# Kernel optimization log

Hardware: AMD Instinct MI355X
Metric: run time of the kernel (lower is better)

## Reference

```python
import jax, jax.numpy as jnp
import numpy as np

D = 512; H = 8; DH = D // H; FFN = 2048; K = 31; N = 4; T = 1024


def _ln(x, g, b):
    m = jnp.mean(x, -1, keepdims=True)
    v = jnp.var(x, -1, keepdims=True)
    return (x - m) * jax.lax.rsqrt(v + 1e-5) * g + b


def _ff(x, g, b, w1, b1, w2, b2):
    h = jax.nn.silu(_ln(x, g, b) @ w1 + b1)
    return 0.5 * (h @ w2 + b2)


def _forward(x, rel_pe, ln1_g, ln1_b, ff1_w1, ff1_b1, ff1_w2, ff1_b2,
             an_g, an_b, wq, bq, wk, bk, wv, bv, wo, bo, pos_w, u, v,
             cn_g, cn_b, pe_w, pe_b, dw_w, dw_b, bn_g, bn_b, pc_w, pc_b,
             ln2_g, ln2_b, ff2_w1, ff2_b1, ff2_w2, ff2_b2, fn_g, fn_b):
    Nb, Tt, _ = x.shape
    # macaron FF 1 (half-step)
    x = x + _ff(x, ln1_g, ln1_b, ff1_w1, ff1_b1, ff1_w2, ff1_b2)

    # RPE multi-head attention (Transformer-XL style)
    xa = _ln(x, an_g, an_b)
    split = lambda m: m.reshape(Nb, Tt, H, DH).transpose(0, 2, 1, 3)  # (N,H,T,dh)
    Q = split(xa @ wq + bq)
    Kk = split(xa @ wk + bk)
    V = split(xa @ wv + bv)
    # content-to-content: (Q+u) K^T
    AC = jnp.einsum('nhtd,nhsd->nhts', Q + u[None, :, None, :], Kk)
    # content-to-position: (Q+v) R^T, then rel-shift gather
    R = (rel_pe @ pos_w).reshape(2 * Tt - 1, H, DH)  # (2T-1,H,dh)
    BD_raw = jnp.einsum('nhtd,phd->nhtp', Q + v[None, :, None, :], R)  # (N,H,T,2T-1)
    idx = jnp.arange(Tt - 1, -1, -1)[None, :] + jnp.arange(Tt)[:, None]  # (T,T): i-j+(T-1)
    BD = jnp.take_along_axis(BD_raw, idx[None, None, :, :], axis=-1)  # (N,H,T,T)
    scores = (AC + BD) * (DH ** -0.5)
    attn = jax.nn.softmax(scores, axis=-1)
    out = jnp.einsum('nhts,nhsd->nthd', attn, V).reshape(Nb, Tt, D)
    x = x + (out @ wo + bo)

    # conv module: LN -> pointwise expand -> GLU -> depthwise conv -> BN(eval) -> SiLU -> pointwise
    c = _ln(x, cn_g, cn_b) @ pe_w + pe_b  # (N,T,2D)
    a, g = jnp.split(c, 2, axis=-1)
    c = a * jax.nn.sigmoid(g)
    c = c.transpose(0, 2, 1)  # (N,D,T)
    c = jax.lax.conv_general_dilated(
        c, dw_w, window_strides=(1,), padding=[(K // 2, K // 2)],
        dimension_numbers=('NCH', 'OIH', 'NCH'), feature_group_count=D)
    c = c + dw_b[None, :, None]
    # BatchNorm1d in eval mode: running_mean=0, running_var=1
    c = c * bn_g[None, :, None] + bn_b[None, :, None]
    c = jax.nn.silu(c).transpose(0, 2, 1) @ pc_w + pc_b
    x = x + c

    # macaron FF 2 + final LN
    x = x + _ff(x, ln2_g, ln2_b, ff2_w1, ff2_b1, ff2_w2, ff2_b2)
    return _ln(x, fn_g, fn_b)


def setup_inputs() -> dict:
    keys = iter(jax.random.split(jax.random.key(0), 64))
    def rn(*shape, s=0.02):
        return jax.random.normal(next(keys), shape, jnp.float32) * s
    inp = {}
    inp['x'] = rn(N, T, D, s=1.0)
    inp['rel_pe'] = rn(2 * T - 1, D, s=1.0)
    inp['ln1_g'] = jnp.ones(D); inp['ln1_b'] = jnp.zeros(D)
    inp['ff1_w1'] = rn(D, FFN); inp['ff1_b1'] = jnp.zeros(FFN)
    inp['ff1_w2'] = rn(FFN, D); inp['ff1_b2'] = jnp.zeros(D)
    inp['an_g'] = jnp.ones(D); inp['an_b'] = jnp.zeros(D)
    inp['wq'] = rn(D, D); inp['bq'] = jnp.zeros(D)
    inp['wk'] = rn(D, D); inp['bk'] = jnp.zeros(D)
    inp['wv'] = rn(D, D); inp['bv'] = jnp.zeros(D)
    inp['wo'] = rn(D, D); inp['bo'] = jnp.zeros(D)
    inp['pos_w'] = rn(D, D)
    inp['u'] = rn(H, DH); inp['v'] = rn(H, DH)
    inp['cn_g'] = jnp.ones(D); inp['cn_b'] = jnp.zeros(D)
    inp['pe_w'] = rn(D, 2 * D); inp['pe_b'] = jnp.zeros(2 * D)
    inp['dw_w'] = rn(D, 1, K); inp['dw_b'] = jnp.zeros(D)
    inp['bn_g'] = jnp.ones(D); inp['bn_b'] = jnp.zeros(D)
    inp['pc_w'] = rn(D, D); inp['pc_b'] = jnp.zeros(D)
    inp['ln2_g'] = jnp.ones(D); inp['ln2_b'] = jnp.zeros(D)
    inp['ff2_w1'] = rn(D, FFN); inp['ff2_b1'] = jnp.zeros(FFN)
    inp['ff2_w2'] = rn(FFN, D); inp['ff2_b2'] = jnp.zeros(D)
    inp['fn_g'] = jnp.ones(D); inp['fn_b'] = jnp.zeros(D)
    return inp


def reference(x, rel_pe, ln1_g, ln1_b, ff1_w1, ff1_b1, ff1_w2, ff1_b2,
              an_g, an_b, wq, bq, wk, bk, wv, bv, wo, bo, pos_w, u, v,
              cn_g, cn_b, pe_w, pe_b, dw_w, dw_b, bn_g, bn_b, pc_w, pc_b,
              ln2_g, ln2_b, ff2_w1, ff2_b1, ff2_w2, ff2_b2, fn_g, fn_b):
    return _forward(x, rel_pe, ln1_g, ln1_b, ff1_w1, ff1_b1, ff1_w2, ff1_b2,
                    an_g, an_b, wq, bq, wk, bk, wv, bv, wo, bo, pos_w, u, v,
                    cn_g, cn_b, pe_w, pe_b, dw_w, dw_b, bn_g, bn_b, pc_w, pc_b,
                    ln2_g, ln2_b, ff2_w1, ff2_b1, ff2_w2, ff2_b2, fn_g, fn_b)
```

## Files before the change

### kernel.cpp

```cpp
#include <hip/hip_runtime.h>
#include <hip/hip_bf16.h>

using bf16 = __hip_bfloat16;
typedef __attribute__((ext_vector_type(8))) short short8;
typedef __attribute__((ext_vector_type(4))) short short4v;
typedef __attribute__((ext_vector_type(4))) float f32x4;

static __device__ __forceinline__ float b2f(bf16 v) { return __bfloat162float(v); }
static __device__ __forceinline__ bf16  f2b(float v) { return __float2bfloat16(v); }
static __device__ __forceinline__ short f2bs(float x) {
    union { float f; unsigned u; } c; c.f = x;
    unsigned r = (c.u + 0x7FFFu + ((c.u >> 16) & 1u)) >> 16;
    return (short)r;
}
static __device__ __forceinline__ float bs2f(short s) {
    union { unsigned u; float f; } c; c.u = ((unsigned)(unsigned short)s) << 16;
    return c.f;
}
static __device__ __forceinline__ void gload16(const short* g, short* l) {
    __builtin_amdgcn_global_load_lds(
        (const __attribute__((address_space(1))) void*)g,
        (__attribute__((address_space(3))) void*)l, 16, 0, 0);
}

constexpr int kD   = 512;
constexpr int kT   = 1024;
constexpr int kN   = 4;
constexpr int kH   = 8;
constexpr int kDH  = 64;
constexpr int kFFN = 2048;
constexpr int kROWS = kN * kT;
constexpr int kP    = 2 * kT - 1;

#define ACT_NONE 0
#define ACT_SILU 1

__global__ __launch_bounds__(256) void stamp_kernel(float* __restrict__ out, int n, float val) {
    int i = blockIdx.x * 256 + threadIdx.x;
    if (i < n) out[i] = (i == 0 ? val : 0.f);
}

__global__ __launch_bounds__(256) void cvt_kernel(const float* __restrict__ in,
                                                  float* __restrict__ out, int n4) {
    int i = blockIdx.x * 256 + threadIdx.x;
    if (i < n4) ((f32x4*)out)[i] = ((const f32x4*)in)[i];
}

struct WtDesc { const float* src; short* dst; int K; int N; int tstart; };
struct WtArgs { WtDesc d[11]; };

__global__ __launch_bounds__(256) void wt_all_kernel(WtArgs a) {
    __shared__ float t[32][33];
    int bid = blockIdx.x;
    int i = 0;
#pragma unroll
    for (int j = 1; j < 11; ++j) if (bid >= a.d[j].tstart) i = j;
    const float* W = a.d[i].src;
    short* Wt = a.d[i].dst;
    int Kd = a.d[i].K, Nd = a.d[i].N;
    int lt = bid - a.d[i].tstart;
    int nx = Nd >> 5;
    int n0 = (lt % nx) * 32, k0 = (lt / nx) * 32;
    int tx = threadIdx.x & 31, ty = threadIdx.x >> 5;
#pragma unroll
    for (int it = 0; it < 4; ++it)
        t[ty + it * 8][tx] = W[(size_t)(k0 + ty + it * 8) * Nd + n0 + tx];
    __syncthreads();
#pragma unroll
    for (int it = 0; it < 4; ++it)
        Wt[(size_t)(n0 + ty + it * 8) * Kd + k0 + tx] = f2bs(t[tx][ty + it * 8]);
}

__global__ __launch_bounds__(256) void vtrans_kernel(const bf16* __restrict__ V,
                                                     bf16* __restrict__ Vt) {
    __shared__ short ts[64][72];
    int tt = blockIdx.x, h = blockIdx.y, n = blockIdx.z;
    int tid = threadIdx.x;
    int r = tid >> 3, cg = (tid & 7) * 8;
#pragma unroll
    for (int it = 0; it < 2; ++it) {
        int row = it * 32 + r;
        *(short8*)&ts[row][cg] =
            *(const short8*)((const short*)V + ((size_t)n * kT + tt * 64 + row) * 512 + h * 64 + cg);
    }
    __syncthreads();
#pragma unroll
    for (int it = 0; it < 2; ++it) {
        int d = it * 32 + r;
        short8 o;
#pragma unroll
        for (int i = 0; i < 8; ++i) o[i] = ts[cg + i][d];
        *(short8*)((short*)Vt + ((size_t)(n * 8 + h) * 64 + d) * 1024 + tt * 64 + cg) = o;
    }
}

__global__ __launch_bounds__(256) void dwt_kernel(const float* __restrict__ dw_w,
                                                  const float* __restrict__ dw_b,
                                                  const float* __restrict__ bn_g,
                                                  const float* __restrict__ bn_b,
                                                  float* __restrict__ wt,
                                                  float* __restrict__ beff) {
    int idx = blockIdx.x * 256 + threadIdx.x;
    if (idx < 31 * kD) {
        int d = idx & 511, k = idx >> 9;
        wt[k * kD + d] = dw_w[d * 31 + k] * bn_g[d];
    }
    if (idx < kD) beff[idx] = dw_b[idx] * bn_g[idx] + bn_b[idx];
}

__global__ __launch_bounds__(256) void ln_kernel_v(const float* __restrict__ xin,
                                                   const float* __restrict__ g,
                                                   const float* __restrict__ b,
                                                   void* __restrict__ outp, int out_f32) {
    int tid = threadIdx.x;
    int rh = tid >> 7;
    int tl = tid & 127;
    int row = blockIdx.x * 2 + rh;
    const float* xr = xin + (size_t)row * kD;
    f32x4 v = *(const f32x4*)(xr + tl * 4);
    float s  = v[0] + v[1] + v[2] + v[3];
    float sq = v[0]*v[0] + v[1]*v[1] + v[2]*v[2] + v[3]*v[3];
    for (int off = 32; off; off >>= 1) {
        s  += __shfl_down(s, off);
        sq += __shfl_down(sq, off);
    }
    __shared__ float ss[4], ssq[4], mean_s[2], rstd_s[2];
    int wid = tid >> 6;
    if ((tid & 63) == 0) { ss[wid] = s; ssq[wid] = sq; }
    __syncthreads();
    if (tid < 2) {
        float S  = ss[tid * 2] + ss[tid * 2 + 1];
        float SQ = ssq[tid * 2] + ssq[tid * 2 + 1];
        float m = S / (float)kD;
        float var = SQ / (float)kD - m * m;
        mean_s[tid] = m;
        rstd_s[tid] = rsqrtf(fmaxf(var, 0.f) + 1e-5f);
    }
    __syncthreads();
    float m = mean_s[rh], rs = rstd_s[rh];
    f32x4 gg = *(const f32x4*)(g + tl * 4);
    f32x4 bb = *(const f32x4*)(b + tl * 4);
    if (out_f32) {
        f32x4 o;
#pragma unroll
        for (int i = 0; i < 4; ++i) o[i] = (v[i] - m) * rs * gg[i] + bb[i];
        *(f32x4*)((float*)outp + (size_t)row * kD + tl * 4) = o;
    } else {
        short4v o;
#pragma unroll
        for (int i = 0; i < 4; ++i) o[i] = f2bs((v[i] - m) * rs * gg[i] + bb[i]);
        *(short4v*)((short*)outp + (size_t)row * kD + tl * 4) = o;
    }
}

__global__ __launch_bounds__(256) void ln_kernel(const float* __restrict__ xin,
                                                 const float* __restrict__ g,
                                                 const float* __restrict__ b,
                                                 void* __restrict__ outp, int out_f32) {
    int row = blockIdx.x;
    const float* xr = xin + (size_t)row * kD;
    int tid = threadIdx.x;
    float v0 = xr[tid], v1 = xr[tid + 256];
    float s = v0 + v1, sq = v0 * v0 + v1 * v1;
    for (int off = 32; off; off >>= 1) {
        s  += __shfl_down(s, off);
        sq += __shfl_down(sq, off);
    }
    __shared__ float ss[4], ssq[4];
    __shared__ float mean_s, rstd_s;
    int wid = tid >> 6, lane = tid & 63;
    if (lane == 0) { ss[wid] = s; ssq[wid] = sq; }
    __syncthreads();
    if (tid == 0) {
        float S  = ss[0] + ss[1] + ss[2] + ss[3];
        float SQ = ssq[0] + ssq[1] + ssq[2] + ssq[3];
        float m = S / (float)kD;
        float var = SQ / (float)kD - m * m;
        mean_s = m;
        rstd_s = rsqrtf(fmaxf(var, 0.f) + 1e-5f);
    }
    __syncthreads();
    float m = mean_s, rs = rstd_s;
    float o0 = (v0 - m) * rs * g[tid]       + b[tid];
    float o1 = (v1 - m) * rs * g[tid + 256] + b[tid + 256];
    size_t i0 = (size_t)row * kD + tid, i1 = i0 + 256;
    if (out_f32) {
        ((float*)outp)[i0] = o0; ((float*)outp)[i1] = o1;
    } else {
        ((bf16*)outp)[i0] = f2b(o0); ((bf16*)outp)[i1] = f2b(o1);
    }
}

__global__ __launch_bounds__(256, 4) void gemm_mfma64(
    const void* __restrict__ A, const short* __restrict__ Bt,
    const float* __restrict__ bias, const float* __restrict__ residual,
    float* __restrict__ outf, bf16* __restrict__ outb,
    int M, int N, int K, int act, float scale, int a_f32) {
    __shared__ short As[2][4096];
    __shared__ short Bs[2][4096];
    int tid = threadIdx.x;
    int m0 = blockIdx.y * 64, n0 = blockIdx.x * 64;
    int wid = tid >> 6, lane = tid & 63;
    int wm = (wid >> 1) * 32, wn = (wid & 1) * 32;
    int q = lane >> 4, c16 = lane & 15;

    f32x4 zero4 = {0.f, 0.f, 0.f, 0.f};
    f32x4 acc[2][2] = {{zero4, zero4}, {zero4, zero4}};

    int arow = lane >> 3;
    int aseg = (lane & 7) ^ arow;

    auto issueA = [&](int buf, int k0) {
        if (!a_f32) {
#pragma unroll
            for (int it = 0; it < 2; ++it) {
                int rbase = (wid * 2 + it) * 8;
                gload16((const short*)A + (size_t)(m0 + rbase + arow) * K + k0 + aseg * 8,
                        &As[buf][(wid * 2 + it) * 512]);
            }
        } else {
            int srow = tid >> 3, sseg = tid & 7;
#pragma unroll
            for (int it = 0; it < 2; ++it) {
                int row = it * 32 + srow;
                int rr = m0 + row;
                short8 v = {0, 0, 0, 0, 0, 0, 0, 0};
                if (rr < M) {
                    const float* ap = (const float*)A + (size_t)rr * K + k0 + sseg * 8;
                    f32x4 x0 = *(const f32x4*)ap;
                    f32x4 x1 = *(const f32x4*)(ap + 4);
                    v[0] = f2bs(x0[0]); v[1] = f2bs(x0[1]); v[2] = f2bs(x0[2]); v[3] = f2bs(x0[3]);
                    v[4] = f2bs(x1[0]); v[5] = f2bs(x1[1]); v[6] = f2bs(x1[2]); v[7] = f2bs(x1[3]);
                }
                *(short8*)&As[buf][(row * 8 + (sseg ^ (row & 7))) * 8] = v;
            }
        }
    };
    auto issueB = [&](int buf, int k0) {
#pragma unroll
        for (int it = 0; it < 2; ++it) {
            int rbase = (wid * 2 + it) * 8;
            gload16(Bt + (size_t)(n0 + rbase + arow) * K + k0 + aseg * 8,
                    &Bs[buf][(wid * 2 + it) * 512]);
        }
    };

    issueA(0, 0);
    issueB(0, 0);
    int cur = 0;
    for (int k0 = 0; k0 < K; k0 += 64) {
        __syncthreads();
        if (k0 + 64 < K) {
            issueA(cur ^ 1, k0 + 64);
            issueB(cur ^ 1, k0 + 64);
        }
#pragma unroll
        for (int ks = 0; ks < 2; ++ks) {
            int p = c16 & 7;
            short8 af[2], bfr[2];
#pragma unroll
            for (int mt = 0; mt < 2; ++mt) {
                int row = wm + mt * 16 + c16;
                af[mt] = *(const short8*)&As[cur][(row * 8 + ((ks * 4 + q) ^ p)) * 8];
            }
#pragma unroll
            for (int nt = 0; nt < 2; ++nt) {
                int row = wn + nt * 16 + c16;
                bfr[nt] = *(const short8*)&Bs[cur][(row * 8 + ((ks * 4 + q) ^ p)) * 8];
            }
#pragma unroll
            for (int mt = 0; mt < 2; ++mt)
#pragma unroll
                for (int nt = 0; nt < 2; ++nt)
                    acc[mt][nt] = __builtin_amdgcn_mfma_f32_16x16x32_bf16(
                        af[mt], bfr[nt], acc[mt][nt], 0, 0, 0);
        }
        cur ^= 1;
    }
#pragma unroll
    for (int mt = 0; mt < 2; ++mt) {
#pragma unroll
        for (int reg = 0; reg < 4; ++reg) {
            int r = m0 + wm + mt * 16 + q * 4 + reg;
            if (r >= M) continue;
#pragma unroll
            for (int nt = 0; nt < 2; ++nt) {
                int c = n0 + wn + nt * 16 + c16;
                float h = acc[mt][nt][reg];
                if (bias) h += bias[c];
                if (act == ACT_SILU) h = h / (1.f + __expf(-h));
                h *= scale;
                size_t idx = (size_t)r * N + c;
                if (residual) h += residual[idx];
                if (outf) outf[idx] = h;
                if (outb) outb[idx] = f2b(h);
            }
        }
    }
}

__global__ __launch_bounds__(256, 4) void gemm_qkv(
    const bf16* __restrict__ A, const short* __restrict__ Bt,
    const float* __restrict__ bq, const float* __restrict__ bk,
    const float* __restrict__ bv,
    bf16* __restrict__ Qb, bf16* __restrict__ Kb, bf16* __restrict__ Vb) {
    const int K = kD;
    __shared__ short As[2][4096];
    __shared__ short Bs[2][4096];
    int tid = threadIdx.x;
    int m0 = blockIdx.y * 64, n0 = blockIdx.x * 64;
    int seg = blockIdx.x >> 3;
    const float* bias = seg == 0 ? bq : (seg == 1 ? bk : bv);
    bf16* outb = seg == 0 ? Qb : (seg == 1 ? Kb : Vb);
    int ns0 = n0 & 511;
    int wid = tid >> 6, lane = tid & 63;
    int wm = (wid >> 1) * 32, wn = (wid & 1) * 32;
    int q = lane >> 4, c16 = lane & 15;

    f32x4 zero4 = {0.f, 0.f, 0.f, 0.f};
    f32x4 acc[2][2] = {{zero4, zero4}, {zero4, zero4}};
    int arow = lane >> 3;
    int aseg = (lane & 7) ^ arow;

    auto issue = [&](int buf, int k0) {
#pragma unroll
        for (int it = 0; it < 2; ++it) {
            int rbase = (wid * 2 + it) * 8;
            gload16((const short*)A + (size_t)(m0 + rbase + arow) * K + k0 + aseg * 8,
                    &As[buf][(wid * 2 + it) * 512]);
            gload16(Bt + (size_t)(n0 + rbase + arow) * K + k0 + aseg * 8,
                    &Bs[buf][(wid * 2 + it) * 512]);
        }
    };

    issue(0, 0);
    int cur = 0;
    for (int k0 = 0; k0 < K; k0 += 64) {
        __syncthreads();
        if (k0 + 64 < K) issue(cur ^ 1, k0 + 64);
#pragma unroll
        for (int ks = 0; ks < 2; ++ks) {
            int p = c16 & 7;
            short8 af[2], bfr[2];
#pragma unroll
            for (int mt = 0; mt < 2; ++mt) {
                int row = wm + mt * 16 + c16;
                af[mt] = *(const short8*)&As[cur][(row * 8 + ((ks * 4 + q) ^ p)) * 8];
            }
#pragma unroll
            for (int nt = 0; nt < 2; ++nt) {
                int row = wn + nt * 16 + c16;
                bfr[nt] = *(const short8*)&Bs[cur][(row * 8 + ((ks * 4 + q) ^ p)) * 8];
            }
#pragma unroll
            for (int mt = 0; mt < 2; ++mt)
#pragma unroll
                for (int nt = 0; nt < 2; ++nt)
                    acc[mt][nt] = __builtin_amdgcn_mfma_f32_16x16x32_bf16(
                        af[mt], bfr[nt], acc[mt][nt], 0, 0, 0);
        }
        cur ^= 1;
    }
#pragma unroll
    for (int mt = 0; mt < 2; ++mt)
#pragma unroll
        for (int reg = 0; reg < 4; ++reg) {
            int r = m0 + wm + mt * 16 + q * 4 + reg;
#pragma unroll
            for (int nt = 0; nt < 2; ++nt) {
                int c = ns0 + wn + nt * 16 + c16;
                outb[(size_t)r * 512 + c] = f2b(acc[mt][nt][reg] + bias[c]);
            }
        }
}

__global__ __launch_bounds__(256) void gemm_scalar(
    const void* __restrict__ A, const float* __restrict__ W,
    const float* __restrict__ bias, const float* __restrict__ residual,
    float* __restrict__ outf, bf16* __restrict__ outb,
    int M, int N, int K, int act, float scale, int a_f32) {
    __shared__ float As[16][65];
    __shared__ float Bs[16][65];
    int tid = threadIdx.x;
    int tx = tid & 15, ty = tid >> 4;
    int row0 = blockIdx.y * 64, col0 = blockIdx.x * 64;
    float acc[4][4] = {};
    for (int k0 = 0; k0 < K; k0 += 16) {
        for (int i = tid; i < 64 * 16; i += 256) {
            int r = i >> 4, c = i & 15;
            int rr = row0 + r;
            float v = 0.f;
            if (rr < M) {
                size_t idx = (size_t)rr * K + k0 + c;
                v = a_f32 ? ((const float*)A)[idx] : b2f(((const bf16*)A)[idx]);
            }
            As[c][r] = v;
        }
        for (int i = tid; i < 16 * 64; i += 256) {
            int r = i >> 6, c = i & 63;
            Bs[r][c] = W[(size_t)(k0 + r) * N + col0 + c];
        }
        __syncthreads();
#pragma unroll
        for (int kk = 0; kk < 16; ++kk) {
            float a[4], b[4];
#pragma unroll
            for (int i = 0; i < 4; ++i) a[i] = As[kk][ty * 4 + i];
#pragma unroll
            for (int j = 0; j < 4; ++j) b[j] = Bs[kk][tx * 4 + j];
#pragma unroll
            for (int i = 0; i < 4; ++i)
#pragma unroll
                for (int j = 0; j < 4; ++j) acc[i][j] += a[i] * b[j];
        }
        __syncthreads();
    }
#pragma unroll
    for (int i = 0; i < 4; ++i) {
        int r = row0 + ty * 4 + i;
        if (r >= M) continue;
#pragma unroll
        for (int j = 0; j < 4; ++j) {
            int c = col0 + tx * 4 + j;
            float h = acc[i][j];
            if (bias) h += bias[c];
            if (act == ACT_SILU) h = h / (1.f + __expf(-h));
            h *= scale;
            size_t idx = (size_t)r * N + c;
            if (residual) h += residual[idx];
            if (outf) outf[idx] = h;
            if (outb) outb[idx] = f2b(h);
        }
    }
}

__global__ __launch_bounds__(256, 2) void attn_mfma(
    const bf16* __restrict__ Qg, const bf16* __restrict__ Kg,
    const bf16* __restrict__ Vtg, const bf16* __restrict__ Rg,
    const float* __restrict__ uu, const float* __restrict__ vvp,
    bf16* __restrict__ outb) {
    __shared__ short Qu[64][72];
    __shared__ short Qv[64][72];
    __shared__ short Ks[64][72];
    __shared__ short Vt[64][72];
    __shared__ short Rw[128][72];
    __shared__ short Bp[64][136];

    int tid = threadIdx.x;
    int qb = blockIdx.x, h = blockIdx.y, n = blockIdx.z;
    int t0 = qb * 64;
    size_t baseq = ((size_t)n * kT) * 512 + (size_t)h * kDH;
    size_t basev = ((size_t)(n * 8 + h) * 64) * 1024;
    size_t baseo = ((size_t)n * kT) * kD + (size_t)h * kDH;

    int wid = tid >> 6, lane = tid & 63;
    int q = lane >> 4, c16 = lane & 15;
    int wm = wid * 16;
    int trow = wm + q * 4;

    {
        int t = tid >> 2, dg = (tid & 3) * 16;
        const short* qp = (const short*)Qg + baseq + (size_t)(t0 + t) * 512 + dg;
        short8 q0 = *(const short8*)qp;
        short8 q1 = *(const short8*)(qp + 8);
#pragma unroll
        for (int i = 0; i < 8; ++i) {
            float qv = bs2f(q0[i]);
            Qu[t][dg + i] = f2bs(qv + uu[h * 64 + dg + i]);
            Qv[t][dg + i] = f2bs(qv + vvp[h * 64 + dg + i]);
        }
#pragma unroll
        for (int i = 0; i < 8; ++i) {
            float qv = bs2f(q1[i]);
            Qu[t][dg + 8 + i] = f2bs(qv + uu[h * 64 + dg + 8 + i]);
            Qv[t][dg + 8 + i] = f2bs(qv + vvp[h * 64 + dg + 8 + i]);
        }
    }

    f32x4 zero4 = {0.f, 0.f, 0.f, 0.f};
    f32x4 acc_o[4] = {zero4, zero4, zero4, zero4};
    float m_i[4] = {-1e30f, -1e30f, -1e30f, -1e30f};
    float l_i[4] = {0.f, 0.f, 0.f, 0.f};

    for (int kt = 0; kt < 16; ++kt) {
        int s0 = kt * 64;
        __syncthreads();
        {
            int s = tid >> 2, dg = (tid & 3) * 16;
            const short* kp = (const short*)Kg + baseq + (size_t)(s0 + s) * 512 + dg;
            *(short8*)&Ks[s][dg]     = *(const short8*)kp;
            *(short8*)&Ks[s][dg + 8] = *(const short8*)(kp + 8);
            const short* vp = (const short*)Vtg + basev + (size_t)s * 1024 + s0 + dg;
            *(short8*)&Vt[s][dg]     = *(const short8*)vp;
            *(short8*)&Vt[s][dg + 8] = *(const short8*)(vp + 8);
        }
        int p_base = t0 - s0 + 960;
#pragma unroll
        for (int it = 0; it < 4; ++it) {
            int i = tid + it * 256;
            int j = i >> 3, dg2 = (i & 7) * 8;
            int p = p_base + j;
            p = p < 0 ? 0 : (p > 2046 ? 2046 : p);
            *(short8*)&Rw[j][dg2] =
                *(const short8*)((const short*)Rg + (size_t)p * kD + h * kDH + dg2);
        }
        __syncthreads();

        f32x4 acc_s[4] = {zero4, zero4, zero4, zero4};
        f32x4 acc_b[5] = {zero4, zero4, zero4, zero4, zero4};
#pragma unroll
        for (int ks = 0; ks < 2; ++ks) {
            short8 au = *(const short8*)&Qu[wm + c16][ks * 32 + q * 8];
            short8 av = *(const short8*)&Qv[wm + c16][ks * 32 + q * 8];
#pragma unroll
            for (int nt = 0; nt < 4; ++nt) {
                short8 bk_ = *(const short8*)&Ks[nt * 16 + c16][ks * 32 + q * 8];
                acc_s[nt] = __builtin_amdgcn_mfma_f32_16x16x32_bf16(au, bk_, acc_s[nt], 0, 0, 0);
            }
#pragma unroll
            for (int jt = 0; jt < 5; ++jt) {
                short8 br_ = *(const short8*)&Rw[wm + jt * 16 + c16][ks * 32 + q * 8];
                acc_b[jt] = __builtin_amdgcn_mfma_f32_16x16x32_bf16(av, br_, acc_b[jt], 0, 0, 0);
            }
        }
#pragma unroll
        for (int jt = 0; jt < 5; ++jt)
#pragma unroll
            for (int reg = 0; reg < 4; ++reg)
                Bp[trow + reg][wm + jt * 16 + c16] = f2bs(acc_b[jt][reg]);

        float pmat[4][4];
        float alpha[4];
#pragma unroll
        for (int reg = 0; reg < 4; ++reg) {
            int t = trow + reg;
            float mrow = -1e30f;
#pragma unroll
            for (int nt = 0; nt < 4; ++nt) {
                int s = nt * 16 + c16;
                int j = t - s + 63;
                float sv = (acc_s[nt][reg] + bs2f(Bp[t][j])) * 0.125f;
                pmat[nt][reg] = sv;
                mrow = fmaxf(mrow, sv);
            }
            mrow = fmaxf(mrow, __shfl_xor(mrow, 1));
            mrow = fmaxf(mrow, __shfl_xor(mrow, 2));
            mrow = fmaxf(mrow, __shfl_xor(mrow, 4));
            mrow = fmaxf(mrow, __shfl_xor(mrow, 8));
            float m_new = fmaxf(m_i[reg], mrow);
            alpha[reg] = __expf(m_i[reg] - m_new);
            float ps = 0.f;
#pragma unroll
            for (int nt = 0; nt < 4; ++nt) {
                float pe = __expf(pmat[nt][reg] - m_new);
                pmat[nt][reg] = pe;
                ps += pe;
            }
            ps += __shfl_xor(ps, 1);
            ps += __shfl_xor(ps, 2);
            ps += __shfl_xor(ps, 4);
            ps += __shfl_xor(ps, 8);
            l_i[reg] = l_i[reg] * alpha[reg] + ps;
            m_i[reg] = m_new;
        }
#pragma unroll
        for (int nt = 0; nt < 4; ++nt)
#pragma unroll
            for (int reg = 0; reg < 4; ++reg)
                Bp[trow + reg][nt * 16 + c16] = f2bs(pmat[nt][reg]);
#pragma unroll
        for (int dt = 0; dt < 4; ++dt)
#pragma unroll
            for (int reg = 0; reg < 4; ++reg)
                acc_o[dt][reg] *= alpha[reg];
#pragma unroll
        for (int ks = 0; ks < 2; ++ks) {
            short8 ap = *(const short8*)&Bp[wm + c16][ks * 32 + q * 8];
#pragma unroll
            for (int dt = 0; dt < 4; ++dt) {
                short8 bv_ = *(const short8*)&Vt[dt * 16 + c16][ks * 32 + q * 8];
                acc_o[dt] = __builtin_amdgcn_mfma_f32_16x16x32_bf16(ap, bv_, acc_o[dt], 0, 0, 0);
            }
        }
    }
#pragma unroll
    for (int reg = 0; reg < 4; ++reg) {
        float inv = 1.f / l_i[reg];
        int t = trow + reg;
#pragma unroll
        for (int dt = 0; dt < 4; ++dt)
            outb[baseo + (size_t)(t0 + t) * kD + dt * 16 + c16] = f2b(acc_o[dt][reg] * inv);
    }
}

__global__ __launch_bounds__(256) void attn_kernel(
    const bf16* __restrict__ Qg, const bf16* __restrict__ Kg,
    const bf16* __restrict__ Vg, const bf16* __restrict__ Rg,
    const float* __restrict__ uu, const float* __restrict__ vvp,
    bf16* __restrict__ outb) {
    __shared__ float Qs[64][65];
    __shared__ bf16 Ps[64][66];
    __shared__ bf16 Ks[64][66];
    __shared__ bf16 Vs[64][66];
    __shared__ bf16 Rs[127][66];
    __shared__ float uf[64], vf[64];
    __shared__ float uK[64], vR[127];

    int tid = threadIdx.x;
    int qb = blockIdx.x, h = blockIdx.y, n = blockIdx.z;
    int t0 = qb * 64;
    size_t base = ((size_t)n * kT) * kD + (size_t)h * kDH;

    if (tid < 64) {
        uf[tid] = uu[h * 64 + tid];
        vf[tid] = vvp[h * 64 + tid];
    }
    for (int i = tid; i < 64 * 64; i += 256) {
        int r = i >> 6, d = i & 63;
        Qs[r][d] = b2f(Qg[base + (size_t)(t0 + r) * kD + d]);
    }
    int r = tid >> 2, seg = tid & 3;
    float m_i = -1e30f, l_i = 0.f;
    float Oa[16];
#pragma unroll
    for (int i = 0; i < 16; ++i) Oa[i] = 0.f;

    for (int kt = 0; kt < 16; ++kt) {
        int s0 = kt * 64;
        __syncthreads();
        for (int i = tid; i < 64 * 64; i += 256) {
            int s = i >> 6, d = i & 63;
            Ks[s][d] = Kg[base + (size_t)(s0 + s) * kD + d];
            Vs[s][d] = Vg[base + (size_t)(s0 + s) * kD + d];
        }
        int p_base = t0 - s0 + 960;
        for (int i = tid; i < 127 * 64; i += 256) {
            int j = i >> 6, d = i & 63;
            int p = p_base + j;
            p = p < 0 ? 0 : (p > 2046 ? 2046 : p);
            Rs[j][d] = Rg[(size_t)p * kD + h * kDH + d];
        }
        __syncthreads();
        if (tid < 64) {
            float s_ = 0.f;
            for (int d = 0; d < 64; ++d) s_ += uf[d] * b2f(Ks[tid][d]);
            uK[tid] = s_;
        } else if (tid < 64 + 127) {
            int j = tid - 64;
            float s_ = 0.f;
            for (int d = 0; d < 64; ++d) s_ += vf[d] * b2f(Rs[j][d]);
            vR[j] = s_;
        }
        __syncthreads();
        float sv[16];
        float smax = -1e30f;
#pragma unroll
        for (int jj = 0; jj < 16; ++jj) {
            int s = seg * 16 + jj;
            int j = r - s + 63;
            float acc = 0.f;
            for (int d = 0; d < 64; ++d)
                acc += Qs[r][d] * (b2f(Ks[s][d]) + b2f(Rs[j][d]));
            acc = (acc + uK[s] + vR[j]) * 0.125f;
            sv[jj] = acc;
            smax = fmaxf(smax, acc);
        }
        smax = fmaxf(smax, __shfl_xor(smax, 1));
        smax = fmaxf(smax, __shfl_xor(smax, 2));
        float m_new = fmaxf(m_i, smax);
        float alpha = __expf(m_i - m_new);
        float psum = 0.f;
#pragma unroll
        for (int jj = 0; jj < 16; ++jj) {
            float p = __expf(sv[jj] - m_new);
            Ps[r][seg * 16 + jj] = f2b(p);
            psum += p;
        }
        psum += __shfl_xor(psum, 1);
        psum += __shfl_xor(psum, 2);
        l_i = l_i * alpha + psum;
        m_i = m_new;
#pragma unroll
        for (int i = 0; i < 16; ++i) Oa[i] *= alpha;
        __syncthreads();
        for (int s = 0; s < 64; ++s) {
            float p = b2f(Ps[r][s]);
#pragma unroll
            for (int dd = 0; dd < 16; ++dd)
                Oa[dd] += p * b2f(Vs[s][seg * 16 + dd]);
        }
    }
    float inv = 1.f / l_i;
#pragma unroll
    for (int dd = 0; dd < 16; ++dd)
        outb[base + (size_t)(t0 + r) * kD + seg * 16 + dd] = f2b(Oa[dd] * inv);
}

__global__ __launch_bounds__(256) void glu_kernel_v(const bf16* __restrict__ c,
                                                    bf16* __restrict__ out) {
    int i8 = (blockIdx.x * 256 + threadIdx.x) * 8;
    int row = i8 >> 9, d = i8 & 511;
    const short* cp = (const short*)c + (size_t)row * 1024;
    short8 a8 = *(const short8*)(cp + d);
    short8 g8 = *(const short8*)(cp + 512 + d);
    short8 o;
#pragma unroll
    for (int i = 0; i < 8; ++i) {
        float a = bs2f(a8[i]), g = bs2f(g8[i]);
        o[i] = f2bs(a / (1.f + __expf(-g)));
    }
    *(short8*)((short*)out + i8) = o;
}

__global__ __launch_bounds__(256) void gluconv_kernel(
    const bf16* __restrict__ cbuf, const float* __restrict__ wt,
    const float* __restrict__ beff, bf16* __restrict__ outb) {
    __shared__ short gsm[94][72];
    __shared__ float wsm[31][64];
    __shared__ float bsm[64];
    int tid = threadIdx.x;
    int dg0 = blockIdx.x * 64;
    int t0  = blockIdx.y * 64;
    int n   = blockIdx.z;

#pragma unroll
    for (int it = 0; it < 3; ++it) {
        int idx = tid + it * 256;
        if (idx < 94 * 8) {
            int row = idx >> 3, cg = (idx & 7) * 8;
            int t = t0 - 15 + row;
            short8 o = {0, 0, 0, 0, 0, 0, 0, 0};
            if ((unsigned)t < (unsigned)kT) {
                const short* cp = (const short*)cbuf + ((size_t)n * kT + t) * 1024 + dg0 + cg;
                short8 a8 = *(const short8*)cp;
                short8 g8 = *(const short8*)(cp + 512);
#pragma unroll
                for (int i = 0; i < 8; ++i)
                    o[i] = f2bs(bs2f(a8[i]) / (1.f + __expf(-bs2f(g8[i]))));
            }
            *(short8*)&gsm[row][cg] = o;
        }
    }
#pragma unroll
    for (int it = 0; it < 8; ++it) {
        int i = tid + it * 256;
        if (i < 31 * 64) wsm[i >> 6][i & 63] = wt[(i >> 6) * kD + dg0 + (i & 63)];
    }
    if (tid < 64) bsm[tid] = beff[dg0 + tid];
    __syncthreads();

    int tl = tid >> 2, dgl = (tid & 3) * 16;
    float acc[16] = {};
#pragma unroll
    for (int k = 0; k < 31; ++k) {
        short8 g0 = *(const short8*)&gsm[tl + k][dgl];
        short8 g1 = *(const short8*)&gsm[tl + k][dgl + 8];
#pragma unroll
        for (int i = 0; i < 8; ++i) {
            acc[i]     += bs2f(g0[i]) * wsm[k][dgl + i];
            acc[8 + i] += bs2f(g1[i]) * wsm[k][dgl + 8 + i];
        }
    }
    short8 o0, o1;
#pragma unroll
    for (int i = 0; i < 8; ++i) {
        float h = acc[i] + bsm[dgl + i];
        o0[i] = f2bs(h / (1.f + __expf(-h)));
        h = acc[8 + i] + bsm[dgl + 8 + i];
        o1[i] = f2bs(h / (1.f + __expf(-h)));
    }
    short* op = (short*)outb + ((size_t)n * kT + t0 + tl) * kD + dg0 + dgl;
    *(short8*)op = o0;
    *(short8*)(op + 8) = o1;
}

__global__ __launch_bounds__(256) void conv_kernel(
    const bf16* __restrict__ glu, const float* __restrict__ dw_w,
    const float* __restrict__ dw_b, const float* __restrict__ bn_g,
    const float* __restrict__ bn_b, bf16* __restrict__ outb) {
    int idx = blockIdx.x * 256 + threadIdx.x;
    int d = idx & 511;
    int t = (idx >> 9) & 1023;
    int n = idx >> 19;
    const bf16* gp = glu + ((size_t)n * kT) * kD + d;
    float acc = 0.f;
#pragma unroll
    for (int k = 0; k < 31; ++k) {
        int tt = t + k - 15;
        if ((unsigned)tt < (unsigned)kT)
            acc += b2f(gp[(size_t)tt * kD]) * dw_w[d * 31 + k];
    }
    acc += dw_b[d];
    acc = acc * bn_g[d] + bn_b[d];
    acc = acc / (1.f + __expf(-acc));
    outb[idx] = f2b(acc);
}

extern "C" void kernel_launch(void* const* d_in, const int* in_sizes, int n_in,
                              void* d_out, int out_size, void* d_ws, size_t ws_size,
                              hipStream_t stream) {
    const float* x      = (const float*)d_in[0];
    const float* rel_pe = (const float*)d_in[1];
    const float* ln1_g  = (const float*)d_in[2];
    const float* ln1_b  = (const float*)d_in[3];
    const float* ff1_w1 = (const float*)d_in[4];
    const float* ff1_b1 = (const float*)d_in[5];
    const float* ff1_w2 = (const float*)d_in[6];
    const float* ff1_b2 = (const float*)d_in[7];
    const float* an_g   = (const float*)d_in[8];
    const float* an_b   = (const float*)d_in[9];
    const float* wq = (const float*)d_in[10]; const float* bq = (const float*)d_in[11];
    const float* wk = (const float*)d_in[12]; const float* bk = (const float*)d_in[13];
    const float* wv = (const float*)d_in[14]; const float* bv = (const float*)d_in[15];
    const float* wo = (const float*)d_in[16]; const float* bo = (const float*)d_in[17];
    const float* pos_w = (const float*)d_in[18];
    const float* uu = (const float*)d_in[19]; const float* vvp = (const float*)d_in[20];
    const float* cn_g = (const float*)d_in[21]; const float* cn_b = (const float*)d_in[22];
    const float* pe_w = (const float*)d_in[23]; const float* pe_b = (const float*)d_in[24];
    const float* dw_w = (const float*)d_in[25]; const float* dw_b = (const float*)d_in[26];
    const float* bn_g = (const float*)d_in[27]; const float* bn_b = (const float*)d_in[28];
    const float* pc_w = (const float*)d_in[29]; const float* pc_b = (const float*)d_in[30];
    const float* ln2_g = (const float*)d_in[31]; const float* ln2_b = (const float*)d_in[32];
    const float* ff2_w1 = (const float*)d_in[33]; const float* ff2_b1 = (const float*)d_in[34];
    const float* ff2_w2 = (const float*)d_in[35]; const float* ff2_b2 = (const float*)d_in[36];
    const float* fn_g = (const float*)d_in[37]; const float* fn_b = (const float*)d_in[38];
    (void)n_in; (void)in_sizes;

    const int total = kROWS * kD;
    dim3 blk(256);
    const size_t MB = 1ull << 20;
    char* w = (char*)d_ws;

    if (ws_size >= 30 * MB) {
        float* xf      = (float*)(w);
        short* ff1_w1t = (short*)(w + 8 * MB);
        short* ff1_w2t = (short*)(w + 10 * MB);
        short* wqt     = (short*)(w + 12 * MB);
        short* wkt     = (short*)(w + 12 * MB + 512 * 1024);
        short* wvt     = (short*)(w + 13 * MB);
        short* wot     = (short*)(w + 13 * MB + 512 * 1024);
        short* poswt   = (short*)(w + 14 * MB);
        short* pewt    = (short*)(w + 14 * MB + 512 * 1024);
        short* pcwt    = (short*)(w + 15 * MB + 512 * 1024);
        short* ff2_w1t = (short*)(w + 16 * MB);
        short* ff2_w2t = (short*)(w + 18 * MB);
        char*  dyn     = w + 20 * MB;
        bf16* hchunk = (bf16*)dyn;
        bf16* Qb     = (bf16*)dyn;
        bf16* Kb     = (bf16*)(dyn + 4 * MB);
        bf16* Rb     = (bf16*)(dyn + 8 * MB);
        bf16* cbuf   = (bf16*)dyn;
        float* dwt   = (float*)(dyn + 8 * MB);
        float* beff  = (float*)(dyn + 8 * MB + 256 * 1024);
        bf16* nb     = (bf16*)d_out;
        bf16* Vtg    = (bf16*)d_out;
        bf16* convb  = (bf16*)d_out;
        bf16* Vb     = (bf16*)d_out + (size_t)kROWS * kD;
        bf16* attnb  = Vb;

        WtArgs wa;
        const float* srcs[11] = {ff1_w1, ff1_w2, wq, wk, wv, wo, pos_w, pe_w, pc_w, ff2_w1, ff2_w2};
        short* dsts[11] = {ff1_w1t, ff1_w2t, wqt, wkt, wvt, wot, poswt, pewt, pcwt, ff2_w1t, ff2_w2t};
        int Ks_[11] = {512, 2048, 512, 512, 512, 512, 512, 512, 512, 512, 2048};
        int Ns_[11] = {2048, 512, 512, 512, 512, 512, 512, 1024, 512, 2048, 512};
        int cum = 0;
        for (int i = 0; i < 11; ++i) {
            wa.d[i].src = srcs[i]; wa.d[i].dst = dsts[i];
            wa.d[i].K = Ks_[i]; wa.d[i].N = Ns_[i]; wa.d[i].tstart = cum;
            cum += (Ns_[i] / 32) * (Ks_[i] / 32);
        }
        wt_all_kernel<<<cum, blk, 0, stream>>>(wa);

        ln_kernel_v<<<kROWS / 2, blk, 0, stream>>>(x, ln1_g, ln1_b, nb, 0);
        for (int c = 0; c < 2; ++c) {
            size_t off = (size_t)c * 2048 * kD;
            gemm_mfma64<<<dim3(kFFN / 64, 2048 / 64), blk, 0, stream>>>(
                nb + off, ff1_w1t, ff1_b1, nullptr, nullptr, hchunk,
                2048, kFFN, kD, ACT_SILU, 1.f, 0);
            gemm_mfma64<<<dim3(kD / 64, 2048 / 64), blk, 0, stream>>>(
                hchunk, ff1_w2t, ff1_b2, x + off, xf + off, nullptr,
                2048, kD, kFFN, ACT_NONE, 0.5f, 0);
        }

        ln_kernel_v<<<kROWS / 2, blk, 0, stream>>>(xf, an_g, an_b, nb, 0);
        gemm_qkv<<<dim3(24, kROWS / 64), blk, 0, stream>>>(
            nb, wqt, bq, bk, bv, Qb, Kb, Vb);
        vtrans_kernel<<<dim3(16, 8, 4), blk, 0, stream>>>(Vb, Vtg);
        gemm_mfma64<<<dim3(kD / 64, (kP + 63) / 64), blk, 0, stream>>>(
            rel_pe, poswt, nullptr, nullptr, nullptr, Rb, kP, kD, kD, ACT_NONE, 1.f, 1);
        attn_mfma<<<dim3(kT / 64, kH, kN), blk, 0, stream>>>(Qb, Kb, Vtg, Rb, uu, vvp, attnb);
        gemm_mfma64<<<dim3(kD / 64, kROWS / 64), blk, 0, stream>>>(
            attnb, wot, bo, xf, xf, nullptr, kROWS, kD, kD, ACT_NONE, 1.f, 0);

        dwt_kernel<<<62, blk, 0, stream>>>(dw_w, dw_b, bn_g, bn_b, dwt, beff);
        ln_kernel_v<<<kROWS / 2, blk, 0, stream>>>(xf, cn_g, cn_b, nb, 0);
        gemm_mfma64<<<dim3(2 * kD / 64, kROWS / 64), blk, 0, stream>>>(
            nb, pewt, pe_b, nullptr, nullptr, cbuf, kROWS, 2 * kD, kD, ACT_NONE, 1.f, 0);
        gluconv_kernel<<<dim3(8, 16, 4), blk, 0, stream>>>(cbuf, dwt, beff, convb);
        gemm_mfma64<<<dim3(kD / 64, kROWS / 64), blk, 0, stream>>>(
            convb, pcwt, pc_b, xf, xf, nullptr, kROWS, kD, kD, ACT_NONE, 1.f, 0);

        ln_kernel_v<<<kROWS / 2, blk, 0, stream>>>(xf, ln2_g, ln2_b, nb, 0);
        for (int c = 0; c < 2; ++c) {
            size_t off = (size_t)c * 2048 * kD;
            gemm_mfma64<<<dim3(kFFN / 64, 2048 / 64), blk, 0, stream>>>(
                nb + off, ff2_w1t, ff2_b1, nullptr, nullptr, hchunk,
                2048, kFFN, kD, ACT_SILU, 1.f, 0);
            gemm_mfma64<<<dim3(kD / 64, 2048 / 64), blk, 0, stream>>>(
                hchunk, ff2_w2t, ff2_b2, xf + off, xf + off, nullptr,
                2048, kD, kFFN, ACT_NONE, 0.5f, 0);
        }

        ln_kernel_v<<<kROWS / 2, blk, 0, stream>>>(xf, fn_g, fn_b, d_out, 1);
        return;
    }

    if (ws_size < 22 * MB) {
        stamp_kernel<<<(out_size + 255) / 256, blk, 0, stream>>>(
            (float*)d_out, out_size, 1000.f + (float)(ws_size / MB));
        return;
    }

    float* xf    = (float*)(w);
    bf16*  hbch  = (bf16*)(w + 8 * MB);
    bf16*  Qb    = (bf16*)(w + 8 * MB);
    bf16*  cbuf  = (bf16*)(w + 8 * MB);
    bf16*  convb = (bf16*)(w + 8 * MB);
    bf16*  Kb    = (bf16*)(w + 12 * MB);
    bf16*  Vb    = (bf16*)(w + 16 * MB);
    bf16*  glub  = (bf16*)(w + 16 * MB);
    bf16*  Rb    = (bf16*)(w + 20 * MB);
    bf16*  nb    = (bf16*)d_out;
    bf16*  attnb = (bf16*)d_out;

    cvt_kernel<<<total / 1024, blk, 0, stream>>>(x, xf, total / 4);

    ln_kernel<<<kROWS, blk, 0, stream>>>(xf, ln1_g, ln1_b, nb, 0);
    for (int c = 0; c < 4; ++c) {
        size_t off = (size_t)c * 1024 * kD;
        gemm_scalar<<<dim3(kFFN / 64, 1024 / 64), blk, 0, stream>>>(
            nb + off, ff1_w1, ff1_b1, nullptr, nullptr, hbch, 1024, kFFN, kD, ACT_SILU, 1.f, 0);
        gemm_scalar<<<dim3(kD / 64, 1024 / 64), blk, 0, stream>>>(
            hbch, ff1_w2, ff1_b2, xf + off, xf + off, nullptr, 1024, kD, kFFN, ACT_NONE, 0.5f, 0);
    }

    ln_kernel<<<kROWS, blk, 0, stream>>>(xf, an_g, an_b, nb, 0);
    gemm_scalar<<<dim3(kD / 64, kROWS / 64), blk, 0, stream>>>(
        nb, wq, bq, nullptr, nullptr, Qb, kROWS, kD, kD, ACT_NONE, 1.f, 0);
    gemm_scalar<<<dim3(kD / 64, kROWS / 64), blk, 0, stream>>>(
        nb, wk, bk, nullptr, nullptr, Kb, kROWS, kD, kD, ACT_NONE, 1.f, 0);
    gemm_scalar<<<dim3(kD / 64, kROWS / 64), blk, 0, stream>>>(
        nb, wv, bv, nullptr, nullptr, Vb, kROWS, kD, kD, ACT_NONE, 1.f, 0);
    gemm_scalar<<<dim3(kD / 64, (kP + 63) / 64), blk, 0, stream>>>(
        rel_pe, pos_w, nullptr, nullptr, nullptr, Rb, kP, kD, kD, ACT_NONE, 1.f, 1);
    attn_kernel<<<dim3(kT / 64, kH, kN), blk, 0, stream>>>(Qb, Kb, Vb, Rb, uu, vvp, attnb);
    gemm_scalar<<<dim3(kD / 64, kROWS / 64), blk, 0, stream>>>(
        attnb, wo, bo, xf, xf, nullptr, kROWS, kD, kD, ACT_NONE, 1.f, 0);

    ln_kernel<<<kROWS, blk, 0, stream>>>(xf, cn_g, cn_b, nb, 0);
    gemm_scalar<<<dim3(2 * kD / 64, kROWS / 64), blk, 0, stream>>>(
        nb, pe_w, pe_b, nullptr, nullptr, cbuf, kROWS, 2 * kD, kD, ACT_NONE, 1.f, 0);
    glu_kernel_v<<<total / 2048, blk, 0, stream>>>(cbuf, glub);
    conv_kernel<<<total / 256, blk, 0, stream>>>(glub, dw_w, dw_b, bn_g, bn_b, convb);
    gemm_scalar<<<dim3(kD / 64, kROWS / 64), blk, 0, stream>>>(
        convb, pc_w, pc_b, xf, xf, nullptr, kROWS, kD, kD, ACT_NONE, 1.f, 0);

    ln_kernel<<<kROWS, blk, 0, stream>>>(xf, ln2_g, ln2_b, nb, 0);
    for (int c = 0; c < 4; ++c) {
        size_t off = (size_t)c * 1024 * kD;
        gemm_scalar<<<dim3(kFFN / 64, 1024 / 64), blk, 0, stream>>>(
            nb + off, ff2_w1, ff2_b1, nullptr, nullptr, hbch, 1024, kFFN, kD, ACT_SILU, 1.f, 0);
        gemm_scalar<<<dim3(kD / 64, 1024 / 64), blk, 0, stream>>>(
            hbch, ff2_w2, ff2_b2, xf + off, xf + off, nullptr, 1024, kD, kFFN, ACT_NONE, 0.5f, 0);
    }

    ln_kernel<<<kROWS, blk, 0, stream>>>(xf, fn_g, fn_b, d_out, 1);
}
```

Before: 495.7 us.

## Use direct global-to-LDS loads with XOR swizzle and register-resident Q in attention

Result: faster. 484.5 us (-2.3%).

```diff
diff --git a/kernel.cpp b/kernel.cpp
--- a/kernel.cpp
+++ b/kernel.cpp
@@ -434,17 +434,15 @@
     }
 }
 
-__global__ __launch_bounds__(256, 2) void attn_mfma(
+__global__ __launch_bounds__(256, 3) void attn_mfma(
     const bf16* __restrict__ Qg, const bf16* __restrict__ Kg,
     const bf16* __restrict__ Vtg, const bf16* __restrict__ Rg,
     const float* __restrict__ uu, const float* __restrict__ vvp,
     bf16* __restrict__ outb) {
-    __shared__ short Qu[64][72];
-    __shared__ short Qv[64][72];
-    __shared__ short Ks[64][72];
-    __shared__ short Vt[64][72];
-    __shared__ short Rw[128][72];
-    __shared__ short Bp[64][136];
+    __shared__ short KsL[4096];
+    __shared__ short VtL[4096];
+    __shared__ short RwL[8192];
+    __shared__ short Bp[64][88];
 
     int tid = threadIdx.x;
     int qb = blockIdx.x, h = blockIdx.y, n = blockIdx.z;
@@ -458,24 +456,25 @@
     int wm = wid * 16;
     int trow = wm + q * 4;
 
+    short8 qu[2], qvv[2];
     {
-        int t = tid >> 2, dg = (tid & 3) * 16;
-        const short* qp = (const short*)Qg + baseq + (size_t)(t0 + t) * 512 + dg;
-        short8 q0 = *(const short8*)qp;
-        short8 q1 = *(const short8*)(qp + 8);
-#pragma unroll
-        for (int i = 0; i < 8; ++i) {
-            float qv = bs2f(q0[i]);
-            Qu[t][dg + i] = f2bs(qv + uu[h * 64 + dg + i]);
-            Qv[t][dg + i] = f2bs(qv + vvp[h * 64 + dg + i]);
-        }
-#pragma unroll
-        for (int i = 0; i < 8; ++i) {
-            float qv = bs2f(q1[i]);
-            Qu[t][dg + 8 + i] = f2bs(qv + uu[h * 64 + dg + 8 + i]);
-            Qv[t][dg + 8 + i] = f2bs(qv + vvp[h * 64 + dg + 8 + i]);
-        }
-    }
+        const short* qp = (const short*)Qg + baseq + (size_t)(t0 + wm + c16) * 512;
+#pragma unroll
+        for (int ks = 0; ks < 2; ++ks) {
+            short8 q8 = *(const short8*)(qp + ks * 32 + q * 8);
+            const float* up = uu + h * 64 + ks * 32 + q * 8;
+            const float* vp = vvp + h * 64 + ks * 32 + q * 8;
+#pragma unroll
+            for (int i = 0; i < 8; ++i) {
+                float xq = bs2f(q8[i]);
+                qu[ks][i]  = f2bs(xq + up[i]);
+                qvv[ks][i] = f2bs(xq + vp[i]);
+            }
+        }
+    }
+
+    int arow = lane >> 3;
+    int aseg = (lane & 7) ^ arow;
 
     f32x4 zero4 = {0.f, 0.f, 0.f, 0.f};
     f32x4 acc_o[4] = {zero4, zero4, zero4, zero4};
@@ -485,24 +484,23 @@
     for (int kt = 0; kt < 16; ++kt) {
         int s0 = kt * 64;
         __syncthreads();
-        {
-            int s = tid >> 2, dg = (tid & 3) * 16;
-            const short* kp = (const short*)Kg + baseq + (size_t)(s0 + s) * 512 + dg;
-            *(short8*)&Ks[s][dg]     = *(const short8*)kp;
-            *(short8*)&Ks[s][dg + 8] = *(const short8*)(kp + 8);
-            const short* vp = (const short*)Vtg + basev + (size_t)s * 1024 + s0 + dg;
-            *(short8*)&Vt[s][dg]     = *(const short8*)vp;
-            *(short8*)&Vt[s][dg + 8] = *(const short8*)(vp + 8);
+#pragma unroll
+        for (int it = 0; it < 2; ++it) {
+            int g = wid * 2 + it;
+            gload16((const short*)Kg + baseq + (size_t)(s0 + g * 8 + arow) * 512 + aseg * 8,
+                    KsL + g * 512);
+            gload16((const short*)Vtg + basev + (size_t)(g * 8 + arow) * 1024 + s0 + aseg * 8,
+                    VtL + g * 512);
         }
         int p_base = t0 - s0 + 960;
 #pragma unroll
         for (int it = 0; it < 4; ++it) {
-            int i = tid + it * 256;
-            int j = i >> 3, dg2 = (i & 7) * 8;
+            int g = wid * 4 + it;
+            int j = g * 8 + arow;
             int p = p_base + j;
             p = p < 0 ? 0 : (p > 2046 ? 2046 : p);
-            *(short8*)&Rw[j][dg2] =
-                *(const short8*)((const short*)Rg + (size_t)p * kD + h * kDH + dg2);
+            gload16((const short*)Rg + (size_t)p * kD + h * kDH + aseg * 8,
+                    RwL + g * 512);
         }
         __syncthreads();
 
@@ -510,24 +508,25 @@
         f32x4 acc_b[5] = {zero4, zero4, zero4, zero4, zero4};
 #pragma unroll
         for (int ks = 0; ks < 2; ++ks) {
-            short8 au = *(const short8*)&Qu[wm + c16][ks * 32 + q * 8];
-            short8 av = *(const short8*)&Qv[wm + c16][ks * 32 + q * 8];
+            int pq = c16 & 7;
 #pragma unroll
             for (int nt = 0; nt < 4; ++nt) {
-                short8 bk_ = *(const short8*)&Ks[nt * 16 + c16][ks * 32 + q * 8];
-                acc_s[nt] = __builtin_amdgcn_mfma_f32_16x16x32_bf16(au, bk_, acc_s[nt], 0, 0, 0);
+                int row = nt * 16 + c16;
+                short8 bk_ = *(const short8*)&KsL[(row * 8 + ((ks * 4 + q) ^ pq)) * 8];
+                acc_s[nt] = __builtin_amdgcn_mfma_f32_16x16x32_bf16(qu[ks], bk_, acc_s[nt], 0, 0, 0);
             }
 #pragma unroll
             for (int jt = 0; jt < 5; ++jt) {
-                short8 br_ = *(const short8*)&Rw[wm + jt * 16 + c16][ks * 32 + q * 8];
-                acc_b[jt] = __builtin_amdgcn_mfma_f32_16x16x32_bf16(av, br_, acc_b[jt], 0, 0, 0);
+                int row = wm + jt * 16 + c16;
+                short8 br_ = *(const short8*)&RwL[(row * 8 + ((ks * 4 + q) ^ pq)) * 8];
+                acc_b[jt] = __builtin_amdgcn_mfma_f32_16x16x32_bf16(qvv[ks], br_, acc_b[jt], 0, 0, 0);
             }
         }
 #pragma unroll
         for (int jt = 0; jt < 5; ++jt)
 #pragma unroll
             for (int reg = 0; reg < 4; ++reg)
-                Bp[trow + reg][wm + jt * 16 + c16] = f2bs(acc_b[jt][reg]);
+                Bp[trow + reg][jt * 16 + c16] = f2bs(acc_b[jt][reg]);
 
         float pmat[4][4];
         float alpha[4];
@@ -538,8 +537,8 @@
 #pragma unroll
             for (int nt = 0; nt < 4; ++nt) {
                 int s = nt * 16 + c16;
-                int j = t - s + 63;
-                float sv = (acc_s[nt][reg] + bs2f(Bp[t][j])) * 0.125f;
+                int jc = t - s + 63 - wm;
+                float sv = (acc_s[nt][reg] + bs2f(Bp[t][jc])) * 0.125f;
                 pmat[nt][reg] = sv;
                 mrow = fmaxf(mrow, sv);
             }
@@ -575,10 +574,12 @@
                 acc_o[dt][reg] *= alpha[reg];
 #pragma unroll
         for (int ks = 0; ks < 2; ++ks) {
+            int pq = c16 & 7;
             short8 ap = *(const short8*)&Bp[wm + c16][ks * 32 + q * 8];
 #pragma unroll
             for (int dt = 0; dt < 4; ++dt) {
-                short8 bv_ = *(const short8*)&Vt[dt * 16 + c16][ks * 32 + q * 8];
+                int row = dt * 16 + c16;
+                short8 bv_ = *(const short8*)&VtL[(row * 8 + ((ks * 4 + q) ^ pq)) * 8];
                 acc_o[dt] = __builtin_amdgcn_mfma_f32_16x16x32_bf16(ap, bv_, acc_o[dt], 0, 0, 0);
             }
         }
```
